# Kernel optimization log

Hardware: AMD Instinct MI355X
Metric: run time of the kernel (lower is better)

Reference implementation:

```python
import jax, jax.numpy as jnp
import numpy as np

B, N, D, H = 2, 2048, 512, 8
MAX_LEN, SEQ = 1000, 2048  # seq_len must equal N for matmul(attn, v)
HD = D // H
BAND = 3


def setup_inputs() -> dict:
    key = jax.random.key(0)
    ks = jax.random.split(key, 12)
    s = 0.02
    return {
        "q": jax.random.normal(ks[0], (B, N, D), jnp.float32),
        "k": jax.random.normal(ks[1], (B, N, D), jnp.float32),
        "v": jax.random.normal(ks[2], (B, N, D), jnp.float32),  # unused by the module
        "Wq": jax.random.normal(ks[3], (D, D), jnp.float32) * s,
        "bq": jnp.zeros((D,), jnp.float32),
        "Wk": jax.random.normal(ks[4], (D, D), jnp.float32) * s,
        "bk": jnp.zeros((D,), jnp.float32),
        "V_emb": jax.random.normal(ks[5], (MAX_LEN, D), jnp.float32),  # nn.Embedding weight
        "Wv2": jax.random.normal(ks[6], (MAX_LEN, SEQ), jnp.float32) * s,  # Linear(max_len, seq_len)
        "bv2": jnp.zeros((SEQ,), jnp.float32),
        "Wout": jax.random.normal(ks[7], (D, D), jnp.float32) * s,
        "bout": jnp.zeros((D,), jnp.float32),
    }


def reference(q, k, v, Wq, bq, Wk, bk, V_emb, Wv2, bv2, Wout, bout):
    b, n, d = q.shape
    qp = q @ Wq + bq                      # [B,N,D]
    kp = k @ Wk + bk                      # [B,N,D]
    # V comes from the embedding table, mixed over the length axis: [seq_len, D]
    v_seq = jnp.einsum('md,ms->sd', V_emb, Wv2) + bv2[:, None]
    qh = qp.reshape(b, n, H, HD).transpose(0, 2, 1, 3)   # [B,H,N,HD]
    kh = kp.reshape(b, n, H, HD).transpose(0, 2, 1, 3)   # [B,H,N,HD]
    vh = v_seq.reshape(n, H, HD).transpose(1, 0, 2)      # [H,N,HD]
    attn = jnp.einsum('bhnd,bhmd->bhnm', qh, kh) / jnp.sqrt(jnp.float32(HD))
    idx = jnp.arange(n)
    band = jnp.abs(idx[:, None] - idx[None, :]) <= BAND  # |i-j|<=3
    # masked_fill(band, -inf): the BAND is excluded from attention (faithful to source)
    attn = jnp.where(band[None, None], -jnp.inf, attn)
    attn = jax.nn.softmax(attn, axis=-1)                 # [B,H,N,N]
    out = jnp.einsum('bhnm,hmd->bhnd', attn, vh)         # [B,H,N,HD]
    out = out.transpose(0, 2, 1, 3).reshape(b, n, d)
    out = out @ Wout + bout
    return out, attn
```

## Files before the change

### kernel.cpp

```cpp
#include <hip/hip_runtime.h>
#include <math.h>

#define BB 2
#define NN 2048
#define DD 512
#define HH 8
#define HD 64
#define KML 1000

typedef long long i64;
typedef unsigned short u16;
typedef __attribute__((ext_vector_type(8))) short bf16x8;
typedef __attribute__((ext_vector_type(16))) float f32x16;

__device__ __forceinline__ u16 f2bf(float x) {
    unsigned int u = __float_as_uint(x);
    u += 0x7FFFu + ((u >> 16) & 1u);
    return (u16)(u >> 16);
}

__global__ __launch_bounds__(256) void tcast5(
    const float* __restrict__ w0, const float* __restrict__ w1,
    const float* __restrict__ w2, const float* __restrict__ w3,
    const float* __restrict__ w4,
    u16* __restrict__ o0, u16* __restrict__ o1, u16* __restrict__ o2,
    u16* __restrict__ o3, u16* __restrict__ o4)
{
    const float* in; u16* out; int K, N, Kp;
    switch (blockIdx.z) {
        case 0: in = w0; out = o0; K = 512;  N = 512;  Kp = 512;  break;
        case 1: in = w1; out = o1; K = 512;  N = 512;  Kp = 512;  break;
        case 2: in = w2; out = o2; K = 512;  N = 512;  Kp = 512;  break;
        case 3: in = w3; out = o3; K = 1000; N = 2048; Kp = 1024; break;
        default:in = w4; out = o4; K = 1000; N = 512;  Kp = 1024; break;
    }
    const int n0 = blockIdx.x * 32, kp0 = blockIdx.y * 32;
    if (n0 >= N || kp0 >= Kp) return;
    __shared__ float ld[32][33];
    const int t = threadIdx.x, tx = t & 31, ty = t >> 5;
#pragma unroll
    for (int i = 0; i < 4; ++i) {
        int kk = kp0 + ty + i * 8;
        ld[ty + i * 8][tx] = (kk < K) ? in[(i64)kk * N + n0 + tx] : 0.f;
    }
    __syncthreads();
#pragma unroll
    for (int i = 0; i < 4; ++i)
        out[(i64)(n0 + ty + i * 8) * Kp + kp0 + tx] = f2bf(ld[tx][ty + i * 8]);
}

template<bool AF32, bool BF16OUT>
__global__ __launch_bounds__(256) void mgemm(
    const void* __restrict__ Ap, const u16* __restrict__ BT,
    const float* __restrict__ bias, void* __restrict__ Cout,
    int M, int N, int K)
{
    __shared__ u16 Asl[64][40];
    __shared__ u16 Bsl[128][40];
    const int t = threadIdx.x;
    const int lane = t & 63, w = t >> 6;
    const int l31 = lane & 31, h5 = lane >> 5;
    const int wm = w >> 1, wn = w & 1;
    const int m0 = blockIdx.y * 64, n0 = blockIdx.x * 128;

    int roff[16];
#pragma unroll
    for (int r = 0; r < 16; ++r) roff[r] = (r & 3) + 8 * (r >> 2) + 4 * h5;

    f32x16 acc[2];
#pragma unroll
    for (int nt = 0; nt < 2; ++nt)
#pragma unroll
        for (int r = 0; r < 16; ++r) acc[nt][r] = 0.f;

    for (int k0 = 0; k0 < K; k0 += 32) {
        __syncthreads();
        {
            int row = t >> 2, kc = (t & 3) * 8;
            if (AF32) {
                const float* A = (const float*)Ap;
                const float* src = A + (i64)(m0 + row) * K + k0 + kc;
                float4 v0 = *(const float4*)src;
                float4 v1 = *(const float4*)(src + 4);
                bf16x8 p;
                p[0] = (short)f2bf(v0.x); p[1] = (short)f2bf(v0.y);
                p[2] = (short)f2bf(v0.z); p[3] = (short)f2bf(v0.w);
                p[4] = (short)f2bf(v1.x); p[5] = (short)f2bf(v1.y);
                p[6] = (short)f2bf(v1.z); p[7] = (short)f2bf(v1.w);
                *(bf16x8*)&Asl[row][kc] = p;
            } else {
                const u16* A = (const u16*)Ap;
                *(bf16x8*)&Asl[row][kc] =
                    *(const bf16x8*)(A + (i64)(m0 + row) * K + k0 + kc);
            }
        }
        {
            int row = t >> 1, kc = (t & 1) * 16;
            const u16* src = BT + (i64)(n0 + row) * K + k0 + kc;
            *(bf16x8*)&Bsl[row][kc]     = *(const bf16x8*)src;
            *(bf16x8*)&Bsl[row][kc + 8] = *(const bf16x8*)(src + 8);
        }
        __syncthreads();
#pragma unroll
        for (int kk = 0; kk < 2; ++kk) {
            bf16x8 af = *(const bf16x8*)&Asl[wm * 32 + l31][kk * 16 + h5 * 8];
#pragma unroll
            for (int nt = 0; nt < 2; ++nt) {
                bf16x8 bf = *(const bf16x8*)&Bsl[wn * 64 + nt * 32 + l31][kk * 16 + h5 * 8];
                acc[nt] = __builtin_amdgcn_mfma_f32_32x32x16_bf16(af, bf, acc[nt], 0, 0, 0);
            }
        }
    }
#pragma unroll
    for (int nt = 0; nt < 2; ++nt) {
        int col = n0 + wn * 64 + nt * 32 + l31;
        float bv = bias[col];
#pragma unroll
        for (int r = 0; r < 16; ++r) {
            int row = m0 + wm * 32 + roff[r];
            float v = acc[nt][r] + bv;
            if (BF16OUT) ((u16*)Cout)[(i64)row * N + col] = f2bf(v);
            else         ((float*)Cout)[(i64)row * N + col] = v;
        }
    }
}

__global__ __launch_bounds__(256, 2) void attn_fused(
    const u16* __restrict__ qbf,
    const u16* __restrict__ kbf,
    const u16* __restrict__ vTb,
    float* __restrict__ attn,
    float* __restrict__ hout)
{
    __shared__ u16   Plds[4][32][40];
    __shared__ float redL[4][32];
    __shared__ float ilsh[32];
    __shared__ float Olds[4][64][36];

    const int t    = threadIdx.x;
    const int lane = t & 63;
    const int w    = t >> 6;
    const int l31  = lane & 31;
    const int h5   = lane >> 5;

    const int bid = blockIdx.x;
    const int swz = (bid & 7) * 128 + (bid >> 3);
    const int bx  = swz & 63;
    const int bh  = swz >> 6;
    const int b   = bh >> 3, h = bh & 7;
    const int i0  = bx * 32;
    const float SC = 0.18033688011112042f;

    const u16* qb = qbf + (i64)(b * NN + i0) * DD + h * HD;
    const u16* kb = kbf + (i64)(b * NN) * DD + h * HD;
    const u16* vb = vTb + (i64)h * HD * NN;
    float* Pg = attn + (i64)bh * NN * NN;

    int roff[16];
#pragma unroll
    for (int r = 0; r < 16; ++r) roff[r] = (r & 3) + 8 * (r >> 2) + 4 * h5;

    bf16x8 qa[4];
#pragma unroll
    for (int f = 0; f < 4; ++f)
        qa[f] = *(const bf16x8*)(qb + (i64)l31 * DD + f * 16 + h5 * 8);

    float lsum[16];
#pragma unroll
    for (int r = 0; r < 16; ++r) lsum[r] = 0.f;

    for (int c = 0; c < 16; ++c) {
        const int j0 = (c * 4 + w) * 32;
        bf16x8 kf[4];
#pragma unroll
        for (int f = 0; f < 4; ++f)
            kf[f] = *(const bf16x8*)(kb + (i64)(j0 + l31) * DD + f * 16 + h5 * 8);
        f32x16 s;
#pragma unroll
        for (int r = 0; r < 16; ++r) s[r] = 0.f;
#pragma unroll
        for (int f = 0; f < 4; ++f)
            s = __builtin_amdgcn_mfma_f32_32x32x16_bf16(qa[f], kf[f], s, 0, 0, 0);
        const int gj = j0 + l31;
        const bool hasband = (j0 >= i0 - 34) && (j0 <= i0 + 34);
        if (hasband) {
#pragma unroll
            for (int r = 0; r < 16; ++r) {
                int d = (i0 + roff[r]) - gj;
                float e = (d >= -3 && d <= 3) ? 0.f
                        : __builtin_amdgcn_exp2f(s[r] * SC);
                lsum[r] += e;
            }
        } else {
#pragma unroll
            for (int r = 0; r < 16; ++r)
                lsum[r] += __builtin_amdgcn_exp2f(s[r] * SC);
        }
    }
#pragma unroll
    for (int r = 0; r < 16; ++r) {
        float v = lsum[r];
        v += __shfl_xor(v, 1);
        v += __shfl_xor(v, 2);
        v += __shfl_xor(v, 4);
        v += __shfl_xor(v, 8);
        v += __shfl_xor(v, 16);
        lsum[r] = v;
    }
    if (l31 == 0) {
#pragma unroll
        for (int r = 0; r < 16; ++r) redL[w][roff[r]] = lsum[r];
    }
    __syncthreads();
    if (t < 32) ilsh[t] = 1.f / (redL[0][t] + redL[1][t] + redL[2][t] + redL[3][t]);
    __syncthreads();
    float ilv[16];
#pragma unroll
    for (int r = 0; r < 16; ++r) ilv[r] = ilsh[roff[r]];

    f32x16 oacc[2];
#pragma unroll
    for (int dt = 0; dt < 2; ++dt)
#pragma unroll
        for (int r = 0; r < 16; ++r) oacc[dt][r] = 0.f;

    for (int c = 0; c < 16; ++c) {
        const int j0 = (c * 4 + w) * 32;
        bf16x8 kf[4];
#pragma unroll
        for (int f = 0; f < 4; ++f)
            kf[f] = *(const bf16x8*)(kb + (i64)(j0 + l31) * DD + f * 16 + h5 * 8);
        f32x16 s;
#pragma unroll
        for (int r = 0; r < 16; ++r) s[r] = 0.f;
#pragma unroll
        for (int f = 0; f < 4; ++f)
            s = __builtin_amdgcn_mfma_f32_32x32x16_bf16(qa[f], kf[f], s, 0, 0, 0);
        const int gj = j0 + l31;
        const bool hasband = (j0 >= i0 - 34) && (j0 <= i0 + 34);
        if (hasband) {
#pragma unroll
            for (int r = 0; r < 16; ++r) {
                int gi = i0 + roff[r];
                int d  = gi - gj;
                float p = (d >= -3 && d <= 3) ? 0.f
                        : __builtin_amdgcn_exp2f(s[r] * SC) * ilv[r];
                Pg[(i64)gi * NN + gj] = p;
                Plds[w][roff[r]][l31] = f2bf(p);
            }
        } else {
#pragma unroll
            for (int r = 0; r < 16; ++r) {
                int gi = i0 + roff[r];
                float p = __builtin_amdgcn_exp2f(s[r] * SC) * ilv[r];
                Pg[(i64)gi * NN + gj] = p;
                Plds[w][roff[r]][l31] = f2bf(p);
            }
        }
#pragma unroll
        for (int jt = 0; jt < 2; ++jt) {
            bf16x8 pa = *(const bf16x8*)&Plds[w][l31][jt * 16 + h5 * 8];
#pragma unroll
            for (int dt = 0; dt < 2; ++dt) {
                bf16x8 vf = *(const bf16x8*)(vb + (i64)(dt * 32 + l31) * NN
                                             + j0 + jt * 16 + h5 * 8);
                oacc[dt] = __builtin_amdgcn_mfma_f32_32x32x16_bf16(pa, vf, oacc[dt], 0, 0, 0);
            }
        }
    }

#pragma unroll
    for (int dt = 0; dt < 2; ++dt) {
        const int d = dt * 32 + l31;
#pragma unroll
        for (int g = 0; g < 4; ++g) {
            float4 o4 = make_float4(oacc[dt][g * 4 + 0], oacc[dt][g * 4 + 1],
                                    oacc[dt][g * 4 + 2], oacc[dt][g * 4 + 3]);
            *(float4*)&Olds[w][d][g * 8 + 4 * h5] = o4;
        }
    }
    __syncthreads();
#pragma unroll
    for (int it = 0; it < 8; ++it) {
        int d = t & 63, row = (t >> 6) + it * 4;
        float v = Olds[0][d][row] + Olds[1][d][row]
                + Olds[2][d][row] + Olds[3][d][row];
        hout[(i64)(b * NN + i0 + row) * DD + h * HD + d] = v;
    }
}

extern "C" void kernel_launch(void* const* d_in, const int* in_sizes, int n_in,
                              void* d_out, int out_size, void* d_ws, size_t ws_size,
                              hipStream_t stream)
{
    const float* q    = (const float*)d_in[0];
    const float* k    = (const float*)d_in[1];
    const float* Wq   = (const float*)d_in[3];
    const float* bq   = (const float*)d_in[4];
    const float* Wk   = (const float*)d_in[5];
    const float* bk   = (const float*)d_in[6];
    const float* Vemb = (const float*)d_in[7];
    const float* Wv2  = (const float*)d_in[8];
    const float* bv2  = (const float*)d_in[9];
    const float* Wout = (const float*)d_in[10];
    const float* bout = (const float*)d_in[11];

    float* outp = (float*)d_out;
    float* attn = outp + (i64)BB * NN * DD;

    u16* qbf   = (u16*)d_ws;
    u16* kbf   = qbf + (i64)4096 * 512;
    u16* vTb   = kbf + (i64)4096 * 512;
    float* hout = (float*)(vTb + (i64)512 * 2048);
    u16* WqT   = (u16*)(hout + (i64)4096 * 512);
    u16* WkT   = WqT + (i64)512 * 512;
    u16* WoT   = WkT + (i64)512 * 512;
    u16* Wv2T  = WoT + (i64)512 * 512;
    u16* VemT  = Wv2T + (i64)2048 * 1024;

    tcast5<<<dim3(64, 32, 5), 256, 0, stream>>>(Wq, Wk, Wout, Wv2, Vemb,
                                                WqT, WkT, WoT, Wv2T, VemT);
    mgemm<true,  true ><<<dim3(4, 64), 256, 0, stream>>>(q, WqT, bq, qbf, 4096, 512, 512);
    mgemm<true,  true ><<<dim3(4, 64), 256, 0, stream>>>(k, WkT, bk, kbf, 4096, 512, 512);
    mgemm<false, true ><<<dim3(16, 8), 256, 0, stream>>>(VemT, Wv2T, bv2, vTb, 512, 2048, 1024);
    attn_fused<<<dim3(1024), 256, 0, stream>>>(qbf, kbf, vTb, attn, hout);
    mgemm<true,  false><<<dim3(4, 64), 256, 0, stream>>>(hout, WoT, bout, outp, 4096, 512, 512);
}
```

Measured before the change: 453.6 us.

## Double-buffer K and V tiles in LDS via async global-to-LDS loads

Both attention passes now stage each 128-column chunk of K (and, in the second pass, the transposed V) into a double-buffered shared-memory pool using global_load_lds. The next chunk is prefetched while the current one is consumed. Fragments are read back through an XOR swizzle meant to avoid bank conflicts. This replaces the per-lane strided global reads of K and V with coalesced asynchronous copies, and the output-reduction scratch now reuses the pool. The cost is a block-wide barrier every chunk and a much larger LDS footprint per block, which may limit residency.

```diff
diff --git a/kernel.cpp b/kernel.cpp
--- a/kernel.cpp
+++ b/kernel.cpp
@@ -17,6 +17,12 @@
     unsigned int u = __float_as_uint(x);
     u += 0x7FFFu + ((u >> 16) & 1u);
     return (u16)(u >> 16);
+}
+
+__device__ __forceinline__ void gload_lds16(const u16* src, const u16* dst) {
+    __builtin_amdgcn_global_load_lds(
+        (const __attribute__((address_space(1))) unsigned int*)src,
+        (__attribute__((address_space(3))) unsigned int*)dst, 16, 0, 0);
 }
 
 __global__ __launch_bounds__(256) void tcast5(
@@ -132,10 +138,11 @@
     float* __restrict__ attn,
     float* __restrict__ hout)
 {
+    __shared__ __align__(16) u16 pool[2][16384];
     __shared__ u16   Plds[4][32][40];
     __shared__ float redL[4][32];
     __shared__ float ilsh[32];
-    __shared__ float Olds[4][64][36];
+    float* Olds = (float*)&pool[0][0];
 
     const int t    = threadIdx.x;
     const int lane = t & 63;
@@ -160,21 +167,51 @@
 #pragma unroll
     for (int r = 0; r < 16; ++r) roff[r] = (r & 3) + 8 * (r >> 2) + 4 * h5;
 
+    auto stageK = [&](int buf, int c) {
+#pragma unroll
+        for (int i = 0; i < 4; ++i) {
+            int e   = i * 64 + lane;
+            int row = w * 32 + (e >> 3);
+            int blk = e & 7;
+            const u16* src = kb + (i64)(c * 128 + row) * DD + ((blk ^ (row & 7)) * 8);
+            const u16* dst = &pool[buf][(w * 256 + i * 64) * 8];
+            gload_lds16(src, dst);
+        }
+    };
+    auto stageV = [&](int buf, int c) {
+#pragma unroll
+        for (int i = 0; i < 4; ++i) {
+            int e  = i * 64 + lane;
+            int d  = w * 16 + (e >> 4);
+            int jb = e & 15;
+            const u16* src = vb + (i64)d * NN + c * 128 + ((jb ^ (d & 15)) * 8);
+            const u16* dst = &pool[buf][8192 + (w * 256 + i * 64) * 8];
+            gload_lds16(src, dst);
+        }
+    };
+
     bf16x8 qa[4];
 #pragma unroll
     for (int f = 0; f < 4; ++f)
         qa[f] = *(const bf16x8*)(qb + (i64)l31 * DD + f * 16 + h5 * 8);
 
+    stageK(0, 0);
+    __syncthreads();
+
     float lsum[16];
 #pragma unroll
     for (int r = 0; r < 16; ++r) lsum[r] = 0.f;
 
     for (int c = 0; c < 16; ++c) {
-        const int j0 = (c * 4 + w) * 32;
+        if (c < 15) stageK((c + 1) & 1, c + 1);
+        const u16* Kc = &pool[c & 1][0];
+        const int j0 = c * 128 + w * 32;
         bf16x8 kf[4];
 #pragma unroll
-        for (int f = 0; f < 4; ++f)
-            kf[f] = *(const bf16x8*)(kb + (i64)(j0 + l31) * DD + f * 16 + h5 * 8);
+        for (int f = 0; f < 4; ++f) {
+            int blk = (f * 2 + h5) ^ (l31 & 7);
+            kf[f] = *(const bf16x8*)&Kc[((w * 32 + l31) * 8 + blk) * 8];
+        }
         f32x16 s;
 #pragma unroll
         for (int r = 0; r < 16; ++r) s[r] = 0.f;
@@ -196,7 +233,12 @@
             for (int r = 0; r < 16; ++r)
                 lsum[r] += __builtin_amdgcn_exp2f(s[r] * SC);
         }
-    }
+        __syncthreads();
+    }
+
+    stageK(0, 0);
+    stageV(0, 0);
+
 #pragma unroll
     for (int r = 0; r < 16; ++r) {
         float v = lsum[r];
@@ -225,11 +267,16 @@
         for (int r = 0; r < 16; ++r) oacc[dt][r] = 0.f;
 
     for (int c = 0; c < 16; ++c) {
-        const int j0 = (c * 4 + w) * 32;
+        if (c < 15) { stageK((c + 1) & 1, c + 1); stageV((c + 1) & 1, c + 1); }
+        const u16* Kc = &pool[c & 1][0];
+        const u16* Vc = &pool[c & 1][8192];
+        const int j0 = c * 128 + w * 32;
         bf16x8 kf[4];
 #pragma unroll
-        for (int f = 0; f < 4; ++f)
-            kf[f] = *(const bf16x8*)(kb + (i64)(j0 + l31) * DD + f * 16 + h5 * 8);
+        for (int f = 0; f < 4; ++f) {
+            int blk = (f * 2 + h5) ^ (l31 & 7);
+            kf[f] = *(const bf16x8*)&Kc[((w * 32 + l31) * 8 + blk) * 8];
+        }
         f32x16 s;
 #pragma unroll
         for (int r = 0; r < 16; ++r) s[r] = 0.f;
@@ -262,11 +309,12 @@
             bf16x8 pa = *(const bf16x8*)&Plds[w][l31][jt * 16 + h5 * 8];
 #pragma unroll
             for (int dt = 0; dt < 2; ++dt) {
-                bf16x8 vf = *(const bf16x8*)(vb + (i64)(dt * 32 + l31) * NN
-                                             + j0 + jt * 16 + h5 * 8);
+                int vblk = (w * 4 + jt * 2 + h5) ^ (l31 & 15);
+                bf16x8 vf = *(const bf16x8*)&Vc[((dt * 32 + l31) * 16 + vblk) * 8];
                 oacc[dt] = __builtin_amdgcn_mfma_f32_32x32x16_bf16(pa, vf, oacc[dt], 0, 0, 0);
             }
         }
+        __syncthreads();
     }
 
 #pragma unroll
@@ -276,15 +324,15 @@
         for (int g = 0; g < 4; ++g) {
             float4 o4 = make_float4(oacc[dt][g * 4 + 0], oacc[dt][g * 4 + 1],
                                     oacc[dt][g * 4 + 2], oacc[dt][g * 4 + 3]);
-            *(float4*)&Olds[w][d][g * 8 + 4 * h5] = o4;
+            *(float4*)&Olds[(w * 64 + d) * 36 + g * 8 + 4 * h5] = o4;
         }
     }
     __syncthreads();
 #pragma unroll
     for (int it = 0; it < 8; ++it) {
         int d = t & 63, row = (t >> 6) + it * 4;
-        float v = Olds[0][d][row] + Olds[1][d][row]
-                + Olds[2][d][row] + Olds[3][d][row];
+        float v = Olds[(0 * 64 + d) * 36 + row] + Olds[(1 * 64 + d) * 36 + row]
+                + Olds[(2 * 64 + d) * 36 + row] + Olds[(3 * 64 + d) * 36 + row];
         hout[(i64)(b * NN + i0 + row) * DD + h * HD + d] = v;
     }
 }
```

Result: faster. 431.4 us (-4.9%).
